# Kernel optimization log

Hardware: AMD Instinct MI355X
Metric: run time of the kernel (lower is better)

## Reference

```python
import jax, jax.numpy as jnp
import numpy as np

B, CIN, CE, CA, N, S = 2, 64, 128, 128, 1024, 32
SCALE = np.sqrt(np.float32(CA))  # scale_mode == 'dimfts'


def _vnlin(W, x):
    # VNLinear: linear map over the channel dim of (B, C, 3, N, S)
    return jnp.einsum('oc,bcdns->bodns', W, x)


def setup_inputs() -> dict:
    key = jax.random.key(0)
    ks = jax.random.split(key, 16)
    def w(k, o, i):
        return (jax.random.normal(k, (o, i), jnp.float32) / np.sqrt(np.float32(i)))
    return {
        'group_xyz': jax.random.normal(ks[0], (B, N, S, 3), jnp.float32),
        'group_fts': jax.random.normal(ks[1], (B, CIN, 3, N, S), jnp.float32),
        'query_xyz': jax.random.normal(ks[2], (B, N, 3), jnp.float32),
        'W_e1': w(ks[3], CE, CIN), 'W_e2': w(ks[4], CE, CE),
        'W_q': w(ks[5], CA, CE), 'W_k': w(ks[6], CA, CE), 'W_v': w(ks[7], CA, CE),
        'W_r1': w(ks[8], 64, 1), 'W_r2': w(ks[9], CA, 64),
        'W_std': w(ks[10], 3, CA),
        'W_f1': w(ks[11], CA, CA * 3), 'b_f1': jax.random.normal(ks[12], (CA,), jnp.float32) * 0.02,
        'W_f2': w(ks[13], CA, CA), 'b_f2': jax.random.normal(ks[14], (CA,), jnp.float32) * 0.02,
    }


def reference(group_xyz, group_fts, query_xyz, W_e1, W_e2, W_q, W_k, W_v,
              W_r1, W_r2, W_std, W_f1, b_f1, W_f2, b_f2):
    # vnn_e: two stacked VNLinear layers
    group_emb = _vnlin(W_e2, _vnlin(W_e1, group_fts))        # (B, CE, 3, N, S)
    query_emb = group_emb[..., :1]                           # (B, CE, 3, N, 1)
    q = _vnlin(W_q, query_emb)                               # (B, CA, 3, N, 1)
    k = _vnlin(W_k, group_emb)                               # (B, CA, 3, N, S)
    v = _vnlin(W_v, group_emb)                               # (B, CA, 3, N, S)

    # positional relation: xyz_rel -> (B, 1, 3, N, S) -> vnn_r
    xyz_rel = group_xyz - query_xyz[:, :, None, :]           # (B, N, S, 3)
    xyz_rel = jnp.transpose(xyz_rel[:, :, :, None, :], (0, 3, 4, 1, 2))  # (B,1,3,N,S)
    pos_rel = _vnlin(W_r2, _vnlin(W_r1, xyz_rel))            # (B, CA, 3, N, S)

    # relation_func == 'sub'
    attn = q - k + pos_rel                                   # (B, CA, 3, N, S)

    # VNStdFeatureLin (dim=5, no frame normalization): z0 = VNLinear(CA->3)
    z0 = _vnlin(W_std, attn)                                 # (B, 3, 3, N, S)
    attn = jnp.einsum('bijns,bjkns->bikns', attn, z0)        # (B, CA, 3, N, S) invariant

    # attn_fwd: 1x1 conv -> ReLU -> 1x1 conv on (B, CA*3, N, S)
    attn = attn.reshape(B, CA * 3, N, S)
    h = jax.nn.relu(jnp.einsum('oc,bcns->bons', W_f1, attn) + b_f1[:, None, None])
    a = jnp.einsum('oc,bcns->bons', W_f2, h) + b_f2[:, None, None]  # (B, CA, N, S)

    a = jax.nn.softmax(a[:, :, None, :, :] / SCALE, axis=-1)  # (B, CA, 1, N, S)
    v = v + pos_rel
    resi = jnp.sum(a * v, axis=-1)                            # (B, CA, 3, N)
    return resi
```

## Files before the change

### kernel.cpp

```cpp
#include <hip/hip_runtime.h>
#include <hip/hip_bf16.h>
#include <math.h>

typedef __hip_bfloat16  bf16;
typedef __hip_bfloat162 bf162;
typedef __attribute__((ext_vector_type(8))) short short8;
typedef __attribute__((ext_vector_type(4))) float f32x4;

#define BB   2
#define CINC 64
#define NN   1024
#define SSS  32
#define NS   (NN * SSS)

#define OFF_QT   0
#define OFF_WR   8192
#define OFF_WE21 8320
#define OFF_KB   16512
#define OFF_VB   20608
#define OFF_F1B  24704
#define OFF_F2B  49280
#define WS_NEED_FLOATS 57472

#define S_ATT_B 0
#define S_FTS_B 26112
#define S_SCR_B 39936
#define S_Q_B   41472
#define S_XYZ_B 43008
#define SMEM_BYTES 43392

__device__ __forceinline__ float bf2f(short s) {
    unsigned int u = ((unsigned int)(unsigned short)s) << 16;
    return __uint_as_float(u);
}
__device__ __forceinline__ short f2bf(float f) {
    bf16 h = __float2bfloat16(f);
    return *reinterpret_cast<short*>(&h);
}
__device__ __forceinline__ unsigned pk2(float a, float b) {
    bf162 p = __float22bfloat162_rn(make_float2(a, b));
    return *reinterpret_cast<unsigned*>(&p);
}

__global__ __launch_bounds__(256) void prep1(const float* __restrict__ We1,
                                             const float* __restrict__ We2,
                                             float* __restrict__ ws) {
    int e = blockIdx.x * 256 + threadIdx.x;
    int o = e >> 6, c = e & 63;
    float acc = 0.f;
    for (int m = 0; m < 128; ++m)
        acc = fmaf(We2[o * 128 + m], We1[m * 64 + c], acc);
    ws[OFF_WE21 + o * 64 + c] = acc;
}

__global__ __launch_bounds__(256) void prep2(const float* __restrict__ Wq,
                                             const float* __restrict__ Wk,
                                             const float* __restrict__ Wv,
                                             const float* __restrict__ Wr1,
                                             const float* __restrict__ Wr2,
                                             const float* __restrict__ Wf1,
                                             const float* __restrict__ Wf2,
                                             float* __restrict__ ws) {
    const float* we21 = ws + OFF_WE21;
    int e = blockIdx.x * 256 + threadIdx.x;
    if (e < 8192) {
        int i = e >> 6, c = e & 63;
        float acc = 0.f;
        for (int o = 0; o < 128; ++o)
            acc = fmaf(Wq[i * 128 + o], we21[o * 64 + c], acc);
        ws[OFF_QT + c * 128 + i] = acc;
    } else if (e < 24576) {
        int le = e - 8192;
        const float* W = (le < 8192) ? Wk : Wv;
        bf16* dst = (bf16*)(ws + ((le < 8192) ? OFF_KB : OFF_VB));
        int li = le & 8191;
        int i = li >> 6, c = li & 63;
        float acc = 0.f;
        for (int o = 0; o < 128; ++o)
            acc = fmaf(W[i * 128 + o], we21[o * 64 + c], acc);
        dst[i * 64 + c] = __float2bfloat16(acc);
    } else if (e < 24704) {
        int i = e - 24576;
        float acc = 0.f;
        for (int m = 0; m < 64; ++m)
            acc = fmaf(Wr2[i * 64 + m], Wr1[m], acc);
        ws[OFF_WR + i] = acc;
    } else if (e < 24704 + 49152) {
        int f = e - 24704;
        int o = f / 384, kp = f - o * 384;
        int c = (kp & 127) * 3 + (kp >> 7);
        ((bf16*)(ws + OFF_F1B))[f] = __float2bfloat16(Wf1[o * 384 + c]);
    } else if (e < 24704 + 49152 + 16384) {
        int f = e - (24704 + 49152);
        ((bf16*)(ws + OFF_F2B))[f] = __float2bfloat16(Wf2[f]);
    }
}

__global__ __launch_bounds__(256, 2) void fused_main(
        const float* __restrict__ gxyz, const float* __restrict__ gfts,
        const float* __restrict__ qxyz, const float* __restrict__ Wstd,
        const float* __restrict__ bf1,  const float* __restrict__ bf2,
        const float* __restrict__ ws,   float* __restrict__ out) {
    extern __shared__ char smc[];
    short* s_att = (short*)(smc + S_ATT_B);
    short* h_t   = s_att;
    short* a_t   = s_att + 4352;
    short* fts_s = (short*)(smc + S_FTS_B);
    float* s_scr = (float*)(smc + S_SCR_B);
    float* s_q   = (float*)(smc + S_Q_B);
    float* s_xyz = (float*)(smc + S_XYZ_B);

    const int t    = threadIdx.x;
    const int bid  = blockIdx.x;
    const int b    = bid >> 10;
    const int n    = bid & 1023;
    const int w    = t >> 6;
    const int lane = t & 63;
    const int quad = lane >> 4;
    const int lq   = lane & 15;
    const int wb   = 32 * w;

    const float* gb = gfts + (size_t)b * (CINC * 3 * NS) + n * SSS;

    for (int l4 = t; l4 < 1536; l4 += 256) {
        int c  = l4 / 24;
        int m4 = (l4 - c * 24) * 4;
        int d  = m4 >> 5, s = m4 & 31;
        float4 f = *(const float4*)(gb + (c * 3 + d) * NS + s);
        fts_s[(m4 + 0) * 72 + c] = f2bf(f.x);
        fts_s[(m4 + 1) * 72 + c] = f2bf(f.y);
        fts_s[(m4 + 2) * 72 + c] = f2bf(f.z);
        fts_s[(m4 + 3) * 72 + c] = f2bf(f.w);
    }
    if (t >= 160) {
        int id = t - 160;
        int d = id >> 5, s = id & 31;
        s_xyz[id] = gxyz[((b * NN + n) * SSS + s) * 3 + d] - qxyz[(b * NN + n) * 3 + d];
    }
    if (t < 128) s_scr[t] = ws[OFF_WR + t];
    __syncthreads();

    if (t < 128) {
        const float* qtw = ws + OFF_QT;
        float q0 = 0.f, q1 = 0.f, q2 = 0.f;
        for (int c = 0; c < 64; ++c) {
            float wq = qtw[c * 128 + t];
            q0 = fmaf(wq, bf2f(fts_s[c]),           q0);
            q1 = fmaf(wq, bf2f(fts_s[32 * 72 + c]), q1);
            q2 = fmaf(wq, bf2f(fts_s[64 * 72 + c]), q2);
        }
        s_q[t * 3 + 0] = q0; s_q[t * 3 + 1] = q1; s_q[t * 3 + 2] = q2;
    }
    __syncthreads();

    f32x4 va[6][2];
    {
        const short* kb = (const short*)(ws + OFF_KB);
        const short* vb = (const short*)(ws + OFF_VB);
        short8 Bk[2][2], Bv[2][2];
        #pragma unroll
        for (int it = 0; it < 2; ++it) {
            int irow = (wb + it * 16 + lq) * 64 + quad * 8;
            Bk[it][0] = *(const short8*)(kb + irow);
            Bk[it][1] = *(const short8*)(kb + irow + 32);
            Bv[it][0] = *(const short8*)(vb + irow);
            Bv[it][1] = *(const short8*)(vb + irow + 32);
        }
        #pragma unroll
        for (int mt = 0; mt < 6; ++mt) {
            const short* ap = fts_s + (mt * 16 + lq) * 72 + quad * 8;
            short8 A0 = *(const short8*)(ap);
            short8 A1 = *(const short8*)(ap + 32);
            int d = mt >> 1;
            #pragma unroll
            for (int it = 0; it < 2; ++it) {
                f32x4 kk = {0.f, 0.f, 0.f, 0.f};
                kk = __builtin_amdgcn_mfma_f32_16x16x32_bf16(A0, Bk[it][0], kk, 0, 0, 0);
                kk = __builtin_amdgcn_mfma_f32_16x16x32_bf16(A1, Bk[it][1], kk, 0, 0, 0);
                f32x4 vv = {0.f, 0.f, 0.f, 0.f};
                vv = __builtin_amdgcn_mfma_f32_16x16x32_bf16(A0, Bv[it][0], vv, 0, 0, 0);
                vv = __builtin_amdgcn_mfma_f32_16x16x32_bf16(A1, Bv[it][1], vv, 0, 0, 0);
                int i = wb + it * 16 + lq;
                float qd  = s_q[i * 3 + d];
                float wri = s_scr[i];
                #pragma unroll
                for (int reg = 0; reg < 4; ++reg) {
                    int m = mt * 16 + quad * 4 + reg;
                    float pos = wri * s_xyz[m];
                    s_att[m * 136 + i] = f2bf(qd - kk[reg] + pos);
                    va[mt][it][reg] = vv[reg] + pos;
                }
            }
        }
    }
    __syncthreads();

    for (int o = t; o < 288; o += 256) {
        int j = o / 96;
        int rem = o - j * 96;
        const float* wrow = Wstd + j * 128;
        const short* ap = s_att + rem * 136;
        float acc = 0.f;
        #pragma unroll 4
        for (int i8 = 0; i8 < 16; ++i8) {
            short8 v8 = *(const short8*)(ap + i8 * 8);
            #pragma unroll
            for (int u = 0; u < 8; ++u)
                acc = fmaf(wrow[i8 * 8 + u], bf2f(v8[u]), acc);
        }
        s_scr[o] = acc;
    }
    __syncthreads();

    for (int u = t; u < 512; u += 256) {
        int s  = u >> 4;
        int i0 = (u & 15) * 8;
        float z[3][3];
        #pragma unroll
        for (int j = 0; j < 3; ++j)
            #pragma unroll
            for (int kk = 0; kk < 3; ++kk)
                z[j][kk] = s_scr[j * 96 + kk * 32 + s];
        float af[3][8];
        #pragma unroll
        for (int j = 0; j < 3; ++j) {
            short8 v8 = *(const short8*)(s_att + (j * 32 + s) * 136 + i0);
            #pragma unroll
            for (int x = 0; x < 8; ++x) af[j][x] = bf2f(v8[x]);
        }
        #pragma unroll
        for (int kk = 0; kk < 3; ++kk) {
            short8 o8;
            #pragma unroll
            for (int x = 0; x < 8; ++x)
                o8[x] = f2bf(af[0][x] * z[0][kk] + af[1][x] * z[1][kk] + af[2][x] * z[2][kk]);
            *(short8*)(s_att + (kk * 32 + s) * 136 + i0) = o8;
        }
    }
    __syncthreads();

    f32x4 eacc[2][2];
    {
        f32x4 zz = {0.f, 0.f, 0.f, 0.f};
        eacc[0][0] = zz; eacc[0][1] = zz; eacc[1][0] = zz; eacc[1][1] = zz;
        const short* f1b = (const short*)(ws + OFF_F1B);
        const short* ab0 = f1b + (wb + lq) * 384 + quad * 8;
        const short* ab1 = ab0 + 16 * 384;
        #pragma unroll 2
        for (int ks = 0; ks < 12; ++ks) {
            int kk = ks >> 2;
            int ic = (ks & 3) * 32 + quad * 8;
            short8 a0 = *(const short8*)(ab0 + ks * 32);
            short8 a1 = *(const short8*)(ab1 + ks * 32);
            const short* bp = s_att + (kk * 32) * 136 + ic;
            short8 b0 = *(const short8*)(bp + lq * 136);
            short8 b1 = *(const short8*)(bp + (lq + 16) * 136);
            eacc[0][0] = __builtin_amdgcn_mfma_f32_16x16x32_bf16(a0, b0, eacc[0][0], 0, 0, 0);
            eacc[0][1] = __builtin_amdgcn_mfma_f32_16x16x32_bf16(a0, b1, eacc[0][1], 0, 0, 0);
            eacc[1][0] = __builtin_amdgcn_mfma_f32_16x16x32_bf16(a1, b0, eacc[1][0], 0, 0, 0);
            eacc[1][1] = __builtin_amdgcn_mfma_f32_16x16x32_bf16(a1, b1, eacc[1][1], 0, 0, 0);
        }
    }
    __syncthreads();

    #pragma unroll
    for (int mt = 0; mt < 2; ++mt) {
        int ob = wb + mt * 16 + quad * 4;
        float4 bb = *(const float4*)(bf1 + ob);
        float bv[4] = {bb.x, bb.y, bb.z, bb.w};
        #pragma unroll
        for (int nt = 0; nt < 2; ++nt) {
            f32x4 c = eacc[mt][nt];
            int s = nt * 16 + lq;
            uint2 pk;
            pk.x = pk2(fmaxf(c[0] + bv[0], 0.f), fmaxf(c[1] + bv[1], 0.f));
            pk.y = pk2(fmaxf(c[2] + bv[2], 0.f), fmaxf(c[3] + bv[3], 0.f));
            *(uint2*)(h_t + s * 136 + ob) = pk;
        }
    }
    __syncthreads();

    {
        f32x4 facc[2][2];
        f32x4 zz = {0.f, 0.f, 0.f, 0.f};
        facc[0][0] = zz; facc[0][1] = zz; facc[1][0] = zz; facc[1][1] = zz;
        const short* f2b = (const short*)(ws + OFF_F2B);
        const short* ab0 = f2b + (wb + lq) * 128 + quad * 8;
        const short* ab1 = ab0 + 16 * 128;
        #pragma unroll 2
        for (int ks = 0; ks < 4; ++ks) {
            int c0 = ks * 32 + quad * 8;
            short8 a0 = *(const short8*)(ab0 + ks * 32);
            short8 a1 = *(const short8*)(ab1 + ks * 32);
            short8 b0 = *(const short8*)(h_t + lq * 136 + c0);
            short8 b1 = *(const short8*)(h_t + (lq + 16) * 136 + c0);
            facc[0][0] = __builtin_amdgcn_mfma_f32_16x16x32_bf16(a0, b0, facc[0][0], 0, 0, 0);
            facc[0][1] = __builtin_amdgcn_mfma_f32_16x16x32_bf16(a0, b1, facc[0][1], 0, 0, 0);
            facc[1][0] = __builtin_amdgcn_mfma_f32_16x16x32_bf16(a1, b0, facc[1][0], 0, 0, 0);
            facc[1][1] = __builtin_amdgcn_mfma_f32_16x16x32_bf16(a1, b1, facc[1][1], 0, 0, 0);
        }
        #pragma unroll
        for (int mt = 0; mt < 2; ++mt) {
            int ob = wb + mt * 16 + quad * 4;
            float4 bb = *(const float4*)(bf2 + ob);
            float bv[4] = {bb.x, bb.y, bb.z, bb.w};
            #pragma unroll
            for (int nt = 0; nt < 2; ++nt) {
                f32x4 c = facc[mt][nt];
                int s = nt * 16 + lq;
                uint2 pk;
                pk.x = pk2(c[0] + bv[0], c[1] + bv[1]);
                pk.y = pk2(c[2] + bv[2], c[3] + bv[3]);
                *(uint2*)(a_t + s * 136 + ob) = pk;
            }
        }
    }
    __syncthreads();

    if (t < 128) {
        float vals[32];
        #pragma unroll
        for (int s = 0; s < 32; ++s) vals[s] = bf2f(a_t[s * 136 + t]);
        float mx = -INFINITY;
        #pragma unroll
        for (int s = 0; s < 32; ++s) mx = fmaxf(mx, vals[s]);
        const float inv = 0.08838834764831845f;
        float sum = 0.f;
        #pragma unroll
        for (int s = 0; s < 32; ++s) { vals[s] = __expf((vals[s] - mx) * inv); sum += vals[s]; }
        float rs = 1.f / sum;
        #pragma unroll
        for (int s = 0; s < 32; ++s) a_t[s * 136 + t] = f2bf(vals[s] * rs);
    }
    __syncthreads();

    {
        float pr[2][3];
        #pragma unroll
        for (int it = 0; it < 2; ++it)
            #pragma unroll
            for (int d = 0; d < 3; ++d) pr[it][d] = 0.f;
        #pragma unroll
        for (int mt = 0; mt < 6; ++mt) {
            int d = mt >> 1;
            #pragma unroll
            for (int it = 0; it < 2; ++it) {
                int i = wb + it * 16 + lq;
                #pragma unroll
                for (int reg = 0; reg < 4; ++reg) {
                    int s = (mt & 1) * 16 + quad * 4 + reg;
                    pr[it][d] = fmaf(bf2f(a_t[s * 136 + i]), va[mt][it][reg], pr[it][d]);
                }
            }
        }
        #pragma unroll
        for (int it = 0; it < 2; ++it)
            #pragma unroll
            for (int d = 0; d < 3; ++d) {
                float v = pr[it][d];
                v += __shfl_xor(v, 16);
                v += __shfl_xor(v, 32);
                if (quad == 0) s_scr[(wb + it * 16 + lq) * 3 + d] = v;
            }
    }
    __syncthreads();

    for (int e = t; e < 384; e += 256)
        out[(b * 384 + e) * NN + n] = s_scr[e];
}

extern "C" void kernel_launch(void* const* d_in, const int* in_sizes, int n_in,
                              void* d_out, int out_size, void* d_ws, size_t ws_size,
                              hipStream_t stream) {
    const float* gxyz = (const float*)d_in[0];
    const float* gfts = (const float*)d_in[1];
    const float* qxyz = (const float*)d_in[2];
    const float* We1  = (const float*)d_in[3];
    const float* We2  = (const float*)d_in[4];
    const float* Wq   = (const float*)d_in[5];
    const float* Wk   = (const float*)d_in[6];
    const float* Wv   = (const float*)d_in[7];
    const float* Wr1  = (const float*)d_in[8];
    const float* Wr2  = (const float*)d_in[9];
    const float* Wstd = (const float*)d_in[10];
    const float* bf1  = (const float*)d_in[12];
    const float* bf2  = (const float*)d_in[14];
    float* out = (float*)d_out;
    float* ws  = (float*)d_ws;

    (void)hipFuncSetAttribute((const void*)fused_main,
                              hipFuncAttributeMaxDynamicSharedMemorySize, SMEM_BYTES);

    prep1<<<32, 256, 0, stream>>>(We1, We2, ws);
    prep2<<<353, 256, 0, stream>>>(Wq, Wk, Wv, Wr1, Wr2,
                                   (const float*)d_in[11], (const float*)d_in[13], ws);
    fused_main<<<BB * NN, 256, SMEM_BYTES, stream>>>(gxyz, gfts, qxyz, Wstd,
                                                     bf1, bf2, ws, out);
}
```

Before: 190.6 us.

## Compute VNStd z0 projection with MFMA and compact shared memory layout

Replaces the scalar per-thread dot-product loop for the W_std projection (3x128 by 96 rows) with bf16 MFMA tiles, where the three weight rows are padded into a 16-row A fragment. It also stores q and the relative xyz in shared memory as bf16, loads W_r directly into registers, and overlaps the scratch buffer with the fts region to reduce the LDS footprint. The aim is to cut the serial FMA work in the z0 step and to lower shared memory use, which may help occupancy. In exchange it adds bf16 rounding of q, xyz and W_std and spends MFMA work on mostly padded rows.

```diff
diff --git a/kernel.cpp b/kernel.cpp
--- a/kernel.cpp
+++ b/kernel.cpp
@@ -24,10 +24,10 @@
 
 #define S_ATT_B 0
 #define S_FTS_B 26112
-#define S_SCR_B 39936
-#define S_Q_B   41472
-#define S_XYZ_B 43008
-#define SMEM_BYTES 43392
+#define S_SCR_B 26112
+#define S_Q_B   39936
+#define S_XYZ_B 40704
+#define SMEM_BYTES 40896
 
 __device__ __forceinline__ float bf2f(short s) {
     unsigned int u = ((unsigned int)(unsigned short)s) << 16;
@@ -102,13 +102,13 @@
         const float* __restrict__ bf1,  const float* __restrict__ bf2,
         const float* __restrict__ ws,   float* __restrict__ out) {
     extern __shared__ char smc[];
-    short* s_att = (short*)(smc + S_ATT_B);
-    short* h_t   = s_att;
-    short* a_t   = s_att + 4352;
-    short* fts_s = (short*)(smc + S_FTS_B);
-    float* s_scr = (float*)(smc + S_SCR_B);
-    float* s_q   = (float*)(smc + S_Q_B);
-    float* s_xyz = (float*)(smc + S_XYZ_B);
+    short* s_att  = (short*)(smc + S_ATT_B);
+    short* h_t    = s_att;
+    short* a_t    = s_att + 4352;
+    short* fts_s  = (short*)(smc + S_FTS_B);
+    float* s_scr  = (float*)(smc + S_SCR_B);
+    short* s_qh   = (short*)(smc + S_Q_B);
+    short* s_xyzh = (short*)(smc + S_XYZ_B);
 
     const int t    = threadIdx.x;
     const int bid  = blockIdx.x;
@@ -135,9 +135,9 @@
     if (t >= 160) {
         int id = t - 160;
         int d = id >> 5, s = id & 31;
-        s_xyz[id] = gxyz[((b * NN + n) * SSS + s) * 3 + d] - qxyz[(b * NN + n) * 3 + d];
-    }
-    if (t < 128) s_scr[t] = ws[OFF_WR + t];
+        s_xyzh[id] = f2bf(gxyz[((b * NN + n) * SSS + s) * 3 + d]
+                          - qxyz[(b * NN + n) * 3 + d]);
+    }
     __syncthreads();
 
     if (t < 128) {
@@ -149,7 +149,9 @@
             q1 = fmaf(wq, bf2f(fts_s[32 * 72 + c]), q1);
             q2 = fmaf(wq, bf2f(fts_s[64 * 72 + c]), q2);
         }
-        s_q[t * 3 + 0] = q0; s_q[t * 3 + 1] = q1; s_q[t * 3 + 2] = q2;
+        s_qh[t * 3 + 0] = f2bf(q0);
+        s_qh[t * 3 + 1] = f2bf(q1);
+        s_qh[t * 3 + 2] = f2bf(q2);
     }
     __syncthreads();
 
@@ -166,6 +168,7 @@
             Bv[it][0] = *(const short8*)(vb + irow);
             Bv[it][1] = *(const short8*)(vb + irow + 32);
         }
+        float wr2[2] = { ws[OFF_WR + wb + lq], ws[OFF_WR + wb + 16 + lq] };
         #pragma unroll
         for (int mt = 0; mt < 6; ++mt) {
             const short* ap = fts_s + (mt * 16 + lq) * 72 + quad * 8;
@@ -181,12 +184,11 @@
                 vv = __builtin_amdgcn_mfma_f32_16x16x32_bf16(A0, Bv[it][0], vv, 0, 0, 0);
                 vv = __builtin_amdgcn_mfma_f32_16x16x32_bf16(A1, Bv[it][1], vv, 0, 0, 0);
                 int i = wb + it * 16 + lq;
-                float qd  = s_q[i * 3 + d];
-                float wri = s_scr[i];
+                float qd = bf2f(s_qh[i * 3 + d]);
                 #pragma unroll
                 for (int reg = 0; reg < 4; ++reg) {
                     int m = mt * 16 + quad * 4 + reg;
-                    float pos = wri * s_xyz[m];
+                    float pos = wr2[it] * bf2f(s_xyzh[m]);
                     s_att[m * 136 + i] = f2bf(qd - kk[reg] + pos);
                     va[mt][it][reg] = vv[reg] + pos;
                 }
@@ -195,20 +197,34 @@
     }
     __syncthreads();
 
-    for (int o = t; o < 288; o += 256) {
-        int j = o / 96;
-        int rem = o - j * 96;
-        const float* wrow = Wstd + j * 128;
-        const short* ap = s_att + rem * 136;
-        float acc = 0.f;
-        #pragma unroll 4
-        for (int i8 = 0; i8 < 16; ++i8) {
-            short8 v8 = *(const short8*)(ap + i8 * 8);
-            #pragma unroll
-            for (int u = 0; u < 8; ++u)
-                acc = fmaf(wrow[i8 * 8 + u], bf2f(v8[u]), acc);
-        }
-        s_scr[o] = acc;
+    {
+        short8 As[4];
+        #pragma unroll
+        for (int kc = 0; kc < 4; ++kc) {
+            short8 a = {0, 0, 0, 0, 0, 0, 0, 0};
+            if (lq < 3) {
+                const float* wp = Wstd + lq * 128 + kc * 32 + quad * 8;
+                float4 w0 = *(const float4*)(wp);
+                float4 w1 = *(const float4*)(wp + 4);
+                a[0] = f2bf(w0.x); a[1] = f2bf(w0.y); a[2] = f2bf(w0.z); a[3] = f2bf(w0.w);
+                a[4] = f2bf(w1.x); a[5] = f2bf(w1.y); a[6] = f2bf(w1.z); a[7] = f2bf(w1.w);
+            }
+            As[kc] = a;
+        }
+        for (int tile = w; tile < 6; tile += 4) {
+            f32x4 acc = {0.f, 0.f, 0.f, 0.f};
+            const short* bp = s_att + (tile * 16 + lq) * 136 + quad * 8;
+            #pragma unroll
+            for (int kc = 0; kc < 4; ++kc) {
+                short8 bfr = *(const short8*)(bp + kc * 32);
+                acc = __builtin_amdgcn_mfma_f32_16x16x32_bf16(As[kc], bfr, acc, 0, 0, 0);
+            }
+            if (quad == 0) {
+                #pragma unroll
+                for (int reg = 0; reg < 3; ++reg)
+                    s_scr[reg * 96 + tile * 16 + lq] = acc[reg];
+            }
+        }
     }
     __syncthreads();
 
```

After: 188.9 us. Within noise of the previous version (-0.8%).
